# Optimization experiments

Measured on AMD Instinct MI355X. Metric: run time of the kernel, lower is better.

Reference implementation:

```python
import jax, jax.numpy as jnp
import numpy as np

NEG_INF = jnp.float32(-9e15)
LEAKY_SLOPE = jnp.float32(0.01)  # torch nn.LeakyReLU default


def setup_inputs() -> dict:
    key = jax.random.key(0)
    k1, k2, k3, k4, k5 = jax.random.split(key, 5)
    B, N, din, draw, T = 128, 10000, 64, 64, 8
    D = din + draw
    x = jax.random.normal(k1, (B, N, din), dtype=jnp.float32)
    raw_x = jax.random.normal(k2, (B, N, draw), dtype=jnp.float32)
    # xavier_uniform with gain=1.414 over (D, 1) fan dims
    bound = 1.414 * float(np.sqrt(6.0 / (D + 1)))
    a = jax.random.uniform(k3, (T, D, 1), dtype=jnp.float32, minval=-bound, maxval=bound)
    adj_mask = jax.random.randint(k4, (N,), 0, 2).astype(jnp.float32)
    type_index = jax.random.randint(k5, (B,), 0, T)
    return {"x": x, "raw_x": raw_x, "a": a, "adj_mask": adj_mask,
            "node_index": 0, "type_index": type_index}


def reference(x, raw_x, a, adj_mask, node_index, type_index):
    B, N, _ = x.shape
    T = a.shape[0]
    # broadcast target node features to all nodes and concat with raw features
    target = x[:, node_index, :]                                   # [B, din]
    concat = jnp.concatenate(
        [jnp.broadcast_to(target[:, None, :], (B, N, target.shape[-1])), raw_x],
        axis=-1)                                                   # [B, N, D]
    # per-type additive attention logits (tiny projection D -> 1 per type)
    e = jnp.einsum('bnd,tdo->btn', concat, a)                      # [B, T, N]
    e = jnp.where(e > 0, e, LEAKY_SLOPE * e)                       # LeakyReLU
    masked = jnp.where(adj_mask[None, None, :] > 0, e, NEG_INF)
    att = jax.nn.softmax(masked, axis=-1) * adj_mask[None, None, :]  # [B, T, N]
    # select the attention row matching each sample's type via one-hot
    onehot = jax.nn.one_hot(type_index, T, dtype=att.dtype)        # [B, T]
    probs = jnp.einsum('btn,bt->bn', att, onehot)                  # [B, N]
    return probs
```

## Files before the change

kernel.cpp:

```cpp
#include <hip/hip_runtime.h>
#include <math.h>

#define NEG_INF_F (-9000000000000000.0f)
#define SLOPE 0.01f

constexpr int B_ = 128, N_ = 10000, DIN = 64, DRAW = 64;
constexpr int CHUNK = 1024;
constexpr int NCHUNK = (N_ + CHUNK - 1) / CHUNK;

__global__ __launch_bounds__(256) void pass1_kernel(
    const float* __restrict__ x, const float* __restrict__ raw_x,
    const float* __restrict__ a, const float* __restrict__ adj,
    const int* __restrict__ node_index, const int* __restrict__ type_index,
    float* __restrict__ e_buf, float* __restrict__ pm, float* __restrict__ ps)
{
    const int b = blockIdx.y;
    const int cblk = blockIdx.x;
    const int tid = threadIdx.x;
    const int wave = tid >> 6;
    const int lane = tid & 63;
    const int r = lane >> 4;
    const int c = lane & 15;
    const int t = type_index[b];

    __shared__ float s_adj[CHUNK];
    __shared__ float s_cb;

    const int n0 = cblk * CHUNK;
    const int n1 = (n0 + CHUNK < N_) ? (n0 + CHUNK) : N_;

    for (int i = tid; i < CHUNK; i += 256) {
        const int n = n0 + i;
        s_adj[i] = (n < N_) ? adj[n] : 0.f;
    }

    if (tid < 64) {
        const int ni = node_index[0];
        float v = x[((size_t)b * N_ + ni) * DIN + tid] * a[t * 128 + tid];
        for (int off = 32; off > 0; off >>= 1) v += __shfl_down(v, off);
        if (tid == 0) s_cb = v;
    }
    __syncthreads();
    const float cb = s_cb;

    const float4 a2 = *(const float4*)(a + t * 128 + 64 + c * 4);

    float m = NEG_INF_F, s = 0.f;

    const float* rxb = raw_x + (size_t)b * N_ * DRAW;

    for (int base = n0 + wave * 8; base < n1; base += 32) {
        const bool has1 = (base + 4) < n1;
        const bool act0 = s_adj[base - n0 + r] > 0.f;
        const bool act1 = has1 && (s_adj[base + 4 - n0 + r] > 0.f);

        float4 v0, v1;
        if (act0) v0 = *(const float4*)(rxb + (size_t)base * DRAW + lane * 4);
        if (act1) v1 = *(const float4*)(rxb + (size_t)(base + 4) * DRAW + lane * 4);

        if (act0) {
            float acc = v0.x * a2.x + v0.y * a2.y + v0.z * a2.z + v0.w * a2.w;
            acc += __shfl_xor(acc, 1);
            acc += __shfl_xor(acc, 2);
            acc += __shfl_xor(acc, 4);
            acc += __shfl_xor(acc, 8);
            float e = cb + acc;
            e = (e > 0.f) ? e : SLOPE * e;
            const float M = fmaxf(m, e);
            s = s * __expf(m - M) + __expf(e - M);
            m = M;
            if (c == 0) e_buf[(size_t)b * N_ + base + r] = e;
        }
        if (act1) {
            float acc = v1.x * a2.x + v1.y * a2.y + v1.z * a2.z + v1.w * a2.w;
            acc += __shfl_xor(acc, 1);
            acc += __shfl_xor(acc, 2);
            acc += __shfl_xor(acc, 4);
            acc += __shfl_xor(acc, 8);
            float e = cb + acc;
            e = (e > 0.f) ? e : SLOPE * e;
            const float M = fmaxf(m, e);
            s = s * __expf(m - M) + __expf(e - M);
            m = M;
            if (c == 0) e_buf[(size_t)b * N_ + base + 4 + r] = e;
        }
    }

    __shared__ float sm[256];
    __shared__ float ss[256];
    sm[tid] = m; ss[tid] = s;
    __syncthreads();
    for (int off = 128; off > 0; off >>= 1) {
        if (tid < off) {
            const float m2 = sm[tid + off], s2 = ss[tid + off];
            const float M = fmaxf(sm[tid], m2);
            ss[tid] = ss[tid] * __expf(sm[tid] - M) + s2 * __expf(m2 - M);
            sm[tid] = M;
        }
        __syncthreads();
    }
    if (tid == 0) {
        pm[b * NCHUNK + cblk] = sm[0];
        ps[b * NCHUNK + cblk] = ss[0] * (1.f / 16.f);
    }
}

__global__ __launch_bounds__(256) void pass3_kernel(
    const float* __restrict__ e_buf, const float* __restrict__ adj,
    const float* __restrict__ pm, const float* __restrict__ ps,
    float* __restrict__ out)
{
    const int b = blockIdx.y;
    const int tid = threadIdx.x;

    __shared__ float sM, sInv;
    if (tid < 16) {
        float m = NEG_INF_F, s = 0.f;
        if (tid < NCHUNK) { m = pm[b * NCHUNK + tid]; s = ps[b * NCHUNK + tid]; }
        for (int off = 8; off > 0; off >>= 1) {
            const float m2 = __shfl_xor(m, off);
            const float s2 = __shfl_xor(s, off);
            const float M = fmaxf(m, m2);
            s = s * __expf(m - M) + s2 * __expf(m2 - M);
            m = M;
        }
        if (tid == 0) { sM = m; sInv = 1.f / s; }
    }
    __syncthreads();
    const float M = sM, inv = sInv;

    const int idx4 = blockIdx.x * 256 + tid;
    if (idx4 >= N_ / 4) return;
    const float4 a4 = ((const float4*)adj)[idx4];
    const float4 e4 = ((const float4*)(e_buf + (size_t)b * N_))[idx4];
    float4 o;
    o.x = (a4.x > 0.f) ? __expf(e4.x - M) * inv : 0.f;
    o.y = (a4.y > 0.f) ? __expf(e4.y - M) * inv : 0.f;
    o.z = (a4.z > 0.f) ? __expf(e4.z - M) * inv : 0.f;
    o.w = (a4.w > 0.f) ? __expf(e4.w - M) * inv : 0.f;
    ((float4*)(out + (size_t)b * N_))[idx4] = o;
}

extern "C" void kernel_launch(void* const* d_in, const int* in_sizes, int n_in,
                              void* d_out, int out_size, void* d_ws, size_t ws_size,
                              hipStream_t stream) {
    const float* x     = (const float*)d_in[0];
    const float* raw_x = (const float*)d_in[1];
    const float* a     = (const float*)d_in[2];
    const float* adj   = (const float*)d_in[3];
    const int* node_index = (const int*)d_in[4];
    const int* type_index = (const int*)d_in[5];
    float* out = (float*)d_out;

    float* e_buf = (float*)d_ws;
    float* pm    = e_buf + (size_t)B_ * N_;
    float* ps    = pm + (size_t)B_ * NCHUNK;

    dim3 g1(NCHUNK, B_);
    pass1_kernel<<<g1, 256, 0, stream>>>(x, raw_x, a, adj, node_index, type_index,
                                         e_buf, pm, ps);
    dim3 g3((N_ / 4 + 255) / 256, B_);
    pass3_kernel<<<g3, 256, 0, stream>>>(e_buf, adj, pm, ps, out);
}
```

Measured before the change: 534.0 us.

## Split softmax into max-only first pass and sum-normalize second pass with unconditional loads

The first pass now computes only a running maximum of the masked logits and stores them with masked entries set to the large negative constant. It drops the online exp/sum rescaling and the adjacency-conditional loads in favour of four unconditional float4 row loads per iteration, and the chunk size is halved. The second pass runs one block per batch row: it reduces the chunk maxima, computes the exponentials and their sum in registers, then normalizes and writes. This is meant to raise memory-level parallelism and cut transcendental work in the streaming pass. The cost is reading all raw_x rows, including masked ones that were previously skipped, and the second pass has only 128 blocks.

Result: slower. 573.3 us (+7.4%).

```diff
diff --git a/kernel.cpp b/kernel.cpp
--- a/kernel.cpp
+++ b/kernel.cpp
@@ -5,14 +5,14 @@
 #define SLOPE 0.01f
 
 constexpr int B_ = 128, N_ = 10000, DIN = 64, DRAW = 64;
-constexpr int CHUNK = 1024;
+constexpr int CHUNK = 512;
 constexpr int NCHUNK = (N_ + CHUNK - 1) / CHUNK;
 
 __global__ __launch_bounds__(256) void pass1_kernel(
     const float* __restrict__ x, const float* __restrict__ raw_x,
     const float* __restrict__ a, const float* __restrict__ adj,
     const int* __restrict__ node_index, const int* __restrict__ type_index,
-    float* __restrict__ e_buf, float* __restrict__ pm, float* __restrict__ ps)
+    float* __restrict__ e_buf, float* __restrict__ pm)
 {
     const int b = blockIdx.y;
     const int cblk = blockIdx.x;
@@ -25,6 +25,7 @@
 
     __shared__ float s_adj[CHUNK];
     __shared__ float s_cb;
+    __shared__ float s_wmax[4];
 
     const int n0 = cblk * CHUNK;
     const int n1 = (n0 + CHUNK < N_) ? (n0 + CHUNK) : N_;
@@ -45,100 +46,128 @@
 
     const float4 a2 = *(const float4*)(a + t * 128 + 64 + c * 4);
 
-    float m = NEG_INF_F, s = 0.f;
+    float m = NEG_INF_F;
 
     const float* rxb = raw_x + (size_t)b * N_ * DRAW;
+    float* eb = e_buf + (size_t)b * N_;
 
-    for (int base = n0 + wave * 8; base < n1; base += 32) {
-        const bool has1 = (base + 4) < n1;
-        const bool act0 = s_adj[base - n0 + r] > 0.f;
-        const bool act1 = has1 && (s_adj[base + 4 - n0 + r] > 0.f);
+    for (int base = n0 + wave * 16; base < n1; base += 64) {
+        const float4 v0 = *(const float4*)(rxb + (size_t)(base +  0) * DRAW + lane * 4);
+        const float4 v1 = *(const float4*)(rxb + (size_t)(base +  4) * DRAW + lane * 4);
+        const float4 v2 = *(const float4*)(rxb + (size_t)(base +  8) * DRAW + lane * 4);
+        const float4 v3 = *(const float4*)(rxb + (size_t)(base + 12) * DRAW + lane * 4);
 
-        float4 v0, v1;
-        if (act0) v0 = *(const float4*)(rxb + (size_t)base * DRAW + lane * 4);
-        if (act1) v1 = *(const float4*)(rxb + (size_t)(base + 4) * DRAW + lane * 4);
-
-        if (act0) {
+        {
             float acc = v0.x * a2.x + v0.y * a2.y + v0.z * a2.z + v0.w * a2.w;
-            acc += __shfl_xor(acc, 1);
-            acc += __shfl_xor(acc, 2);
-            acc += __shfl_xor(acc, 4);
-            acc += __shfl_xor(acc, 8);
+            acc += __shfl_xor(acc, 1); acc += __shfl_xor(acc, 2);
+            acc += __shfl_xor(acc, 4); acc += __shfl_xor(acc, 8);
             float e = cb + acc;
             e = (e > 0.f) ? e : SLOPE * e;
-            const float M = fmaxf(m, e);
-            s = s * __expf(m - M) + __expf(e - M);
-            m = M;
-            if (c == 0) e_buf[(size_t)b * N_ + base + r] = e;
+            e = (s_adj[base - n0 + 0 + r] > 0.f) ? e : NEG_INF_F;
+            m = fmaxf(m, e);
+            if (c == 0) eb[base + 0 + r] = e;
         }
-        if (act1) {
+        {
             float acc = v1.x * a2.x + v1.y * a2.y + v1.z * a2.z + v1.w * a2.w;
-            acc += __shfl_xor(acc, 1);
-            acc += __shfl_xor(acc, 2);
-            acc += __shfl_xor(acc, 4);
-            acc += __shfl_xor(acc, 8);
+            acc += __shfl_xor(acc, 1); acc += __shfl_xor(acc, 2);
+            acc += __shfl_xor(acc, 4); acc += __shfl_xor(acc, 8);
             float e = cb + acc;
             e = (e > 0.f) ? e : SLOPE * e;
-            const float M = fmaxf(m, e);
-            s = s * __expf(m - M) + __expf(e - M);
-            m = M;
-            if (c == 0) e_buf[(size_t)b * N_ + base + 4 + r] = e;
+            e = (s_adj[base - n0 + 4 + r] > 0.f) ? e : NEG_INF_F;
+            m = fmaxf(m, e);
+            if (c == 0) eb[base + 4 + r] = e;
+        }
+        {
+            float acc = v2.x * a2.x + v2.y * a2.y + v2.z * a2.z + v2.w * a2.w;
+            acc += __shfl_xor(acc, 1); acc += __shfl_xor(acc, 2);
+            acc += __shfl_xor(acc, 4); acc += __shfl_xor(acc, 8);
+            float e = cb + acc;
+            e = (e > 0.f) ? e : SLOPE * e;
+            e = (s_adj[base - n0 + 8 + r] > 0.f) ? e : NEG_INF_F;
+            m = fmaxf(m, e);
+            if (c == 0) eb[base + 8 + r] = e;
+        }
+        {
+            float acc = v3.x * a2.x + v3.y * a2.y + v3.z * a2.z + v3.w * a2.w;
+            acc += __shfl_xor(acc, 1); acc += __shfl_xor(acc, 2);
+            acc += __shfl_xor(acc, 4); acc += __shfl_xor(acc, 8);
+            float e = cb + acc;
+            e = (e > 0.f) ? e : SLOPE * e;
+            e = (s_adj[base - n0 + 12 + r] > 0.f) ? e : NEG_INF_F;
+            m = fmaxf(m, e);
+            if (c == 0) eb[base + 12 + r] = e;
         }
     }
 
-    __shared__ float sm[256];
-    __shared__ float ss[256];
-    sm[tid] = m; ss[tid] = s;
+    for (int off = 32; off > 0; off >>= 1) m = fmaxf(m, __shfl_xor(m, off));
+    if (lane == 0) s_wmax[wave] = m;
     __syncthreads();
-    for (int off = 128; off > 0; off >>= 1) {
-        if (tid < off) {
-            const float m2 = sm[tid + off], s2 = ss[tid + off];
-            const float M = fmaxf(sm[tid], m2);
-            ss[tid] = ss[tid] * __expf(sm[tid] - M) + s2 * __expf(m2 - M);
-            sm[tid] = M;
-        }
-        __syncthreads();
-    }
     if (tid == 0) {
-        pm[b * NCHUNK + cblk] = sm[0];
-        ps[b * NCHUNK + cblk] = ss[0] * (1.f / 16.f);
+        pm[b * NCHUNK + cblk] =
+            fmaxf(fmaxf(s_wmax[0], s_wmax[1]), fmaxf(s_wmax[2], s_wmax[3]));
     }
 }
 
-__global__ __launch_bounds__(256) void pass3_kernel(
-    const float* __restrict__ e_buf, const float* __restrict__ adj,
-    const float* __restrict__ pm, const float* __restrict__ ps,
+__global__ __launch_bounds__(256) void pass2_kernel(
+    const float* __restrict__ e_buf, const float* __restrict__ pm,
     float* __restrict__ out)
 {
-    const int b = blockIdx.y;
+    const int b = blockIdx.x;
     const int tid = threadIdx.x;
+    const int lane = tid & 63;
+    const int wave = tid >> 6;
 
     __shared__ float sM, sInv;
-    if (tid < 16) {
-        float m = NEG_INF_F, s = 0.f;
-        if (tid < NCHUNK) { m = pm[b * NCHUNK + tid]; s = ps[b * NCHUNK + tid]; }
-        for (int off = 8; off > 0; off >>= 1) {
-            const float m2 = __shfl_xor(m, off);
-            const float s2 = __shfl_xor(s, off);
-            const float M = fmaxf(m, m2);
-            s = s * __expf(m - M) + s2 * __expf(m2 - M);
-            m = M;
-        }
-        if (tid == 0) { sM = m; sInv = 1.f / s; }
+    __shared__ float s_red[4];
+
+    float m = NEG_INF_F;
+    if (tid < NCHUNK) m = pm[b * NCHUNK + tid];
+    if (tid < 64) {
+        for (int off = 32; off > 0; off >>= 1) m = fmaxf(m, __shfl_down(m, off));
+        if (tid == 0) sM = m;
     }
     __syncthreads();
-    const float M = sM, inv = sInv;
+    const float M = sM;
 
-    const int idx4 = blockIdx.x * 256 + tid;
-    if (idx4 >= N_ / 4) return;
-    const float4 a4 = ((const float4*)adj)[idx4];
-    const float4 e4 = ((const float4*)(e_buf + (size_t)b * N_))[idx4];
-    float4 o;
-    o.x = (a4.x > 0.f) ? __expf(e4.x - M) * inv : 0.f;
-    o.y = (a4.y > 0.f) ? __expf(e4.y - M) * inv : 0.f;
-    o.z = (a4.z > 0.f) ? __expf(e4.z - M) * inv : 0.f;
-    o.w = (a4.w > 0.f) ? __expf(e4.w - M) * inv : 0.f;
-    ((float4*)(out + (size_t)b * N_))[idx4] = o;
+    const float4* e4 = (const float4*)(e_buf + (size_t)b * N_);
+    float4* o4 = (float4*)(out + (size_t)b * N_);
+    constexpr int NV = N_ / 4;
+
+    float4 vals[10];
+    float s = 0.f;
+#pragma unroll
+    for (int k = 0; k < 10; ++k) {
+        const int idx = tid + k * 256;
+        if (idx < NV) {
+            float4 v = e4[idx];
+            v.x = __expf(v.x - M);
+            v.y = __expf(v.y - M);
+            v.z = __expf(v.z - M);
+            v.w = __expf(v.w - M);
+            vals[k] = v;
+            s += v.x + v.y + v.z + v.w;
+        }
+    }
+
+    for (int off = 32; off > 0; off >>= 1) s += __shfl_down(s, off);
+    if (lane == 0) s_red[wave] = s;
+    __syncthreads();
+    if (tid == 0) {
+        const float tot = s_red[0] + s_red[1] + s_red[2] + s_red[3];
+        sInv = 1.f / tot;
+    }
+    __syncthreads();
+    const float inv = sInv;
+
+#pragma unroll
+    for (int k = 0; k < 10; ++k) {
+        const int idx = tid + k * 256;
+        if (idx < NV) {
+            float4 v = vals[k];
+            v.x *= inv; v.y *= inv; v.z *= inv; v.w *= inv;
+            o4[idx] = v;
+        }
+    }
 }
 
 extern "C" void kernel_launch(void* const* d_in, const int* in_sizes, int n_in,
@@ -154,11 +183,9 @@
 
     float* e_buf = (float*)d_ws;
     float* pm    = e_buf + (size_t)B_ * N_;
-    float* ps    = pm + (size_t)B_ * NCHUNK;
 
     dim3 g1(NCHUNK, B_);
     pass1_kernel<<<g1, 256, 0, stream>>>(x, raw_x, a, adj, node_index, type_index,
-                                         e_buf, pm, ps);
-    dim3 g3((N_ / 4 + 255) / 256, B_);
-    pass3_kernel<<<g3, 256, 0, stream>>>(e_buf, adj, pm, ps, out);
+                                         e_buf, pm);
+    pass2_kernel<<<dim3(B_), 256, 0, stream>>>(e_buf, pm, out);
 }
```
